# Performance work log

Measured on AMD Instinct MI355X. Metric: run time of the kernel, lower is better.

The kernel has to match this reference:

```python
import jax, jax.numpy as jnp
import numpy as np

B, S, D, H = 4, 2048, 1024, 16
HD = D // H  # head_dim = 64


def setup_inputs() -> dict:
    key = jax.random.key(0)
    k1, k2, k3 = jax.random.split(key, 3)
    x = jax.random.normal(k1, (B, S, D), dtype=jnp.float32)
    W_attn = jax.random.normal(k2, (D, 3 * D), dtype=jnp.float32) * (1.0 / np.sqrt(D))
    b_attn = jnp.zeros((3 * D,), dtype=jnp.float32)
    W_proj = jax.random.normal(k3, (D, D), dtype=jnp.float32) * (1.0 / np.sqrt(D))
    b_proj = jnp.zeros((D,), dtype=jnp.float32)
    return {"x": x, "W_attn": W_attn, "b_attn": b_attn, "W_proj": W_proj, "b_proj": b_proj}


def reference(x, W_attn, b_attn, W_proj, b_proj):
    bsz, seq_len, d = x.shape
    n_head = H
    head_dim = d // n_head
    qkv = x @ W_attn + b_attn                      # [B,S,3D]
    q, k, v = jnp.split(qkv, 3, axis=-1)           # each [B,S,D]
    # -> [B,H,S,hd]
    q = q.reshape(bsz, seq_len, n_head, head_dim).transpose(0, 2, 1, 3)
    k = k.reshape(bsz, seq_len, n_head, head_dim).transpose(0, 2, 1, 3)
    v = v.reshape(bsz, seq_len, n_head, head_dim).transpose(0, 2, 1, 3)
    scale = 1.0 / np.sqrt(head_dim).astype(np.float32)
    att = jnp.einsum("bhqd,bhkd->bhqk", q, k) * scale  # [B,H,S,S]
    causal = jnp.tril(jnp.ones((seq_len, seq_len), dtype=bool))
    att = jnp.where(causal[None, None], att, jnp.float32(-jnp.inf))
    att = jax.nn.softmax(att, axis=-1)
    y = jnp.einsum("bhqk,bhkd->bhqd", att, v)       # [B,H,S,hd]
    y = y.transpose(0, 2, 1, 3).reshape(bsz, seq_len, d)
    return y @ W_proj + b_proj
```

## Files before the change

kernel.cpp:

```cpp
#include <hip/hip_runtime.h>

typedef __attribute__((ext_vector_type(8))) short short8;
typedef __attribute__((ext_vector_type(8))) __bf16 bf16x8;
typedef __attribute__((ext_vector_type(2))) __bf16 bf16x2;
typedef __attribute__((ext_vector_type(4))) float f32x4;
typedef __attribute__((ext_vector_type(2))) unsigned int uint2v;

#define LOG2E 1.44269504088896340736f

__device__ __forceinline__ unsigned short f2b(float f) {
  unsigned u = __builtin_bit_cast(unsigned, f);
  u += 0x7fffu + ((u >> 16) & 1u);
  return (unsigned short)(u >> 16);
}
__device__ __forceinline__ float b2f(unsigned short s) {
  unsigned u = (unsigned)s << 16;
  return __builtin_bit_cast(float, u);
}
__device__ __forceinline__ bf16x8 asbf(short8 s) { return __builtin_bit_cast(bf16x8, s); }

__device__ __forceinline__ void gl_lds16(const void* g, void* l) {
  __builtin_amdgcn_global_load_lds(
      (const __attribute__((address_space(1))) void*)g,
      (__attribute__((address_space(3))) void*)l, 16, 0, 0);
}

__device__ __forceinline__ unsigned lds_a(const void* p) {
  return (unsigned)(size_t)(__attribute__((address_space(3))) const void*)p;
}

__device__ __forceinline__ unsigned pk_bf16(float a, float b) {
  bf16x2 v;
  v[0] = (__bf16)a;
  v[1] = (__bf16)b;
  return __builtin_bit_cast(unsigned, v);
}

template <int N>
__device__ __forceinline__ void wait_vm() {
  if constexpr (N == 7) asm volatile("s_waitcnt vmcnt(7)" ::: "memory");
  else if constexpr (N == 6) asm volatile("s_waitcnt vmcnt(6)" ::: "memory");
  else if constexpr (N == 5) asm volatile("s_waitcnt vmcnt(5)" ::: "memory");
  else asm volatile("s_waitcnt vmcnt(0)" ::: "memory");
}

__global__ void k_cvt_bf16(const float* __restrict__ x, unsigned short* __restrict__ o, int n) {
  int i = (blockIdx.x * 256 + threadIdx.x) * 4;
  if (i >= n) return;
  float4 v = *(const float4*)(x + i);
  ushort4 r;
  r.x = f2b(v.x); r.y = f2b(v.y); r.z = f2b(v.z); r.w = f2b(v.w);
  *(ushort4*)(o + i) = r;
}

__global__ void k_transpose_bf16(const float* __restrict__ W, unsigned short* __restrict__ Wt,
                                 int R, int C) {
  __shared__ float tile[64][65];
  const int tc = blockIdx.x, tr = blockIdx.y;
  const int r0 = tr * 64, c0 = tc * 64;
  for (int it = 0; it < 16; ++it) {
    int lin = it * 256 + threadIdx.x;
    int r = lin >> 6, c = lin & 63;
    tile[r][c] = W[(size_t)(r0 + r) * C + c0 + c];
  }
  __syncthreads();
  for (int it = 0; it < 16; ++it) {
    int lin = it * 256 + threadIdx.x;
    int orr = lin >> 6, oc = lin & 63;
    Wt[(size_t)(c0 + orr) * R + r0 + oc] = f2b(tile[oc][orr]);
  }
}

template <int BNW, bool OUT_BF16>
__global__ __launch_bounds__(512)
void k_gemm256(const unsigned short* __restrict__ A, const unsigned short* __restrict__ Bt,
               const float* __restrict__ bias, void* __restrict__ Cp,
               int M, int N, int K) {
  constexpr int BN = BNW * 4;
  constexpr int NR = BNW / 16;
  __shared__ unsigned short lds[2][(256 + BN) * 64];

  const int tid = threadIdx.x;
  const int wv = tid >> 6, lane = tid & 63;
  const int g = lane >> 4, l15 = lane & 15;
  const int wr = wv >> 2, wc = wv & 3;

  const int ntn = N / BN;
  const int nwg = gridDim.x;
  const int bid = blockIdx.x;
  const int cpx = nwg >> 3;
  const int swz = (bid & 7) * cpx + (bid >> 3);
  const int tm = swz / ntn, tn = swz % ntn;

  const unsigned short* Ab = A + (size_t)(tm * 256) * K;
  const unsigned short* Bb = Bt + (size_t)(tn * BN) * K;

  const int NT = K >> 6, NI = NT >> 1;

  auto As = [&](int buf) -> char* { return (char*)&lds[buf][0]; };
  auto Bs = [&](int buf) -> char* { return (char*)&lds[buf][256 * 64]; };

  auto stageB = [&](int buf, int t) {
#pragma unroll
    for (int it = 0; it < NR; ++it) {
      int cidx = it * 8 + wv;
      int row = cidx * 8 + (lane >> 3);
      int sc = (lane & 7) ^ (row & 7);
      gl_lds16(Bb + (size_t)row * K + t * 64 + sc * 8, Bs(buf) + cidx * 1024 + lane * 16);
    }
  };
  auto stageA = [&](int buf, int t, int q) {
    int row0 = (wv < 4) ? (q * 32 + wv * 8) : (128 + q * 32 + (wv - 4) * 8);
    int row = row0 + (lane >> 3);
    int sc = (lane & 7) ^ (row & 7);
    gl_lds16(Ab + (size_t)row * K + t * 64 + sc * 8, As(buf) + row0 * 128 + lane * 16);
  };

  auto rdA = [&](int buf, int q, int ms, int kh) -> short8 {
    int row = wr * 128 + q * 32 + ms * 16 + l15;
    int ch = (kh * 4 + g) ^ (row & 7);
    return *(const short8*)(As(buf) + row * 128 + ch * 16);
  };
  auto rdB = [&](int buf, int n, int kh) -> short8 {
    int row = wc * BNW + n * 16 + l15;
    int ch = (kh * 4 + g) ^ (row & 7);
    return *(const short8*)(Bs(buf) + row * 128 + ch * 16);
  };

  f32x4 acc[8][NR] = {};
  short8 bfr[NR][2];

  stageB(0, 0);
#pragma unroll
  for (int q = 0; q < 4; ++q) stageA(0, 0, q);
  stageB(1, 1);
#pragma unroll
  for (int q = 0; q < 3; ++q) stageA(1, 1, q);
  wait_vm<NR + 3>();
  __builtin_amdgcn_s_barrier();

  for (int i = 0; i < NI; ++i) {
    const int t0 = 2 * i;
#pragma unroll
    for (int half = 0; half < 2; ++half) {
#pragma unroll
      for (int q = 0; q < 4; ++q) {
        short8 afr[2][2];
#pragma unroll
        for (int ms = 0; ms < 2; ++ms)
#pragma unroll
          for (int kh = 0; kh < 2; ++kh) afr[ms][kh] = rdA(half, q, ms, kh);
        if (q == 0) {
#pragma unroll
          for (int n = 0; n < NR; ++n)
#pragma unroll
            for (int kh = 0; kh < 2; ++kh) bfr[n][kh] = rdB(half, n, kh);
        }
        if (half == 0) {
          if (q == 0) stageA(1, t0 + 1, 3);
          if (q == 1 && t0 + 2 < NT) { stageB(0, t0 + 2); stageA(0, t0 + 2, 0); }
          if (q == 2 && t0 + 2 < NT) stageA(0, t0 + 2, 1);
          if (q == 3 && t0 + 2 < NT) stageA(0, t0 + 2, 2);
        } else {
          if (q == 0 && t0 + 2 < NT) stageA(0, t0 + 2, 3);
          if (q == 1 && t0 + 3 < NT) stageB(1, t0 + 3);
          if (q == 2 && t0 + 3 < NT) stageA(1, t0 + 3, 0);
          if (q == 3 && t0 + 3 < NT) { stageA(1, t0 + 3, 1); stageA(1, t0 + 3, 2); }
        }
        __builtin_amdgcn_s_barrier();
        asm volatile("s_waitcnt lgkmcnt(0)" ::: "memory");
        __builtin_amdgcn_sched_barrier(0);
        __builtin_amdgcn_s_setprio(1);
#pragma unroll
        for (int n = 0; n < NR; ++n)
#pragma unroll
          for (int ms = 0; ms < 2; ++ms)
#pragma unroll
            for (int kh = 0; kh < 2; ++kh)
              acc[q * 2 + ms][n] = __builtin_amdgcn_mfma_f32_16x16x32_bf16(
                  asbf(afr[ms][kh]), asbf(bfr[n][kh]), acc[q * 2 + ms][n], 0, 0, 0);
        __builtin_amdgcn_s_setprio(0);
        if (q == 3) {
          const bool more = (half == 0) ? (t0 + 2 < NT) : (t0 + 3 < NT);
          if (more) wait_vm<NR + 3>();
          else      wait_vm<0>();
        }
        __builtin_amdgcn_s_barrier();
      }
    }
  }

  const int crow0 = tm * 256 + wr * 128 + g * 4;
  const int ccol0 = tn * BN + wc * BNW + l15;
#pragma unroll
  for (int n = 0; n < NR; ++n) {
    int col = ccol0 + n * 16;
    float bv = bias[col];
#pragma unroll
    for (int mq = 0; mq < 8; ++mq)
#pragma unroll
      for (int j = 0; j < 4; ++j) {
        int row = crow0 + mq * 16 + j;
        float v = acc[mq][n][j] + bv;
        if constexpr (OUT_BF16)
          ((unsigned short*)Cp)[(size_t)row * N + col] = f2b(v);
        else
          ((float*)Cp)[(size_t)row * N + col] = v;
      }
  }
}

__global__ __launch_bounds__(512)
void k_attn(const unsigned short* __restrict__ qkv, unsigned short* __restrict__ y) {
  constexpr int SEQ = 2048, TD = 3072, DM = 1024;
  __shared__ unsigned short Kl[2][4096];
  __shared__ unsigned short Vl[2][4096];
  __shared__ unsigned short Pl[8][2048];

  const int f = blockIdx.x;
  const int bh = (f & 7) * 8 + ((f >> 3) & 7);
  const int a = (f >> 6) & 7;
  const int qt = (f < 256) ? (7 - a) : (a - 4);
  const int b = bh >> 4, h = bh & 15;
  const int tid = threadIdx.x;
  const int lane = tid & 63, w = tid >> 6;
  const int g = lane >> 4, l15 = lane & 15;

  const size_t base = (size_t)b * SEQ * TD + h * 64;
  const unsigned short* Kg0 = qkv + base + 1024;
  const unsigned short* Vg0 = qkv + base + 2048;

  short8 onesb;
#pragma unroll
  for (int i = 0; i < 8; ++i) onesb[i] = (short)0x3F80;

  auto stage = [&](int buf, int c) {
    const unsigned short* Kg = Kg0 + (size_t)(c * 64) * TD;
    const unsigned short* Vg = Vg0 + (size_t)(c * 64) * TD;
    const int j = tid;
    int r = j >> 3, cc = j & 7;
    int cck = cc ^ (r & 7);
    gl_lds16(Kg + (size_t)r * TD + cck * 8, (char*)Kl[buf] + j * 16);
    int kv = ((j >> 1) & 3) | (((j >> 5) & 1) << 2) | (((j >> 3) & 3) << 3) |
             (((j >> 6) & 1) << 5);
    int d0 = ((j >> 7) << 4) | ((j & 1) << 3);
    gl_lds16(Vg + (size_t)kv * TD + d0, (char*)Vl[buf] + j * 16);
  };

  char* pw = (char*)Pl + w * 4096;

  const int q0 = qt * 256;
  const int qw = w * 32;

  short8 qf[2][2];
#pragma unroll
  for (int qg = 0; qg < 2; ++qg) {
    const unsigned short* qrow = qkv + base + (size_t)(q0 + qw + qg * 16 + l15) * TD;
#pragma unroll
    for (int kh = 0; kh < 2; ++kh) {
      short8 t = *(const short8*)(qrow + kh * 32 + g * 8);
#pragma unroll
      for (int i = 0; i < 8; ++i)
        t[i] = (short)f2b(b2f((unsigned short)t[i]) * (0.125f * LOG2E));
      qf[qg][kh] = t;
    }
  }

  f32x4 o[2][4] = {};
  f32x4 ol[2] = {};

  const int nch = 4 * (qt + 1);
  int cur = 0;
  stage(0, 0);
  for (int c = 0; c < nch; ++c) {
    if (c + 1 < nch) {
      stage(cur ^ 1, c + 1);
      asm volatile("s_waitcnt vmcnt(2)" ::: "memory");
    } else {
      asm volatile("s_waitcnt vmcnt(0)" ::: "memory");
    }
    __builtin_amdgcn_s_barrier();

    f32x4 sv[2][4];
    __builtin_amdgcn_s_setprio(1);
#pragma unroll
    for (int ff = 0; ff < 4; ++ff) {
      int kv = ff * 16 + l15;
      short8 kf0 = *(const short8*)((const char*)Kl[cur] + kv * 128 + ((g) ^ (kv & 7)) * 16);
      short8 kf1 = *(const short8*)((const char*)Kl[cur] + kv * 128 + ((4 + g) ^ (kv & 7)) * 16);
#pragma unroll
      for (int qg = 0; qg < 2; ++qg) {
        f32x4 s = {};
        s = __builtin_amdgcn_mfma_f32_16x16x32_bf16(asbf(kf0), asbf(qf[qg][0]), s, 0, 0, 0);
        s = __builtin_amdgcn_mfma_f32_16x16x32_bf16(asbf(kf1), asbf(qf[qg][1]), s, 0, 0, 0);
        sv[qg][ff] = s;
      }
    }
    __builtin_amdgcn_s_setprio(0);

    const int crel = c - 4 * qt;
    if (crel >= 0) {
#pragma unroll
      for (int qg = 0; qg < 2; ++qg)
#pragma unroll
        for (int ff = 0; ff < 4; ++ff)
#pragma unroll
          for (int r = 0; r < 4; ++r)
            if (crel * 64 + ff * 16 + g * 4 + r > qw + qg * 16 + l15)
              sv[qg][ff][r] = -128.f;
    }

#pragma unroll
    for (int qg = 0; qg < 2; ++qg)
#pragma unroll
      for (int ff = 0; ff < 4; ++ff) {
        float p0 = __builtin_amdgcn_exp2f(sv[qg][ff][0]);
        float p1 = __builtin_amdgcn_exp2f(sv[qg][ff][1]);
        float p2 = __builtin_amdgcn_exp2f(sv[qg][ff][2]);
        float p3 = __builtin_amdgcn_exp2f(sv[qg][ff][3]);
        unsigned w0 = pk_bf16(p0, p1);
        unsigned w1 = pk_bf16(p2, p3);
        unsigned long long pk = (unsigned long long)w0 | ((unsigned long long)w1 << 32);
        int off = qg * 2048 + ((l15 * 128 + ff * 32 + g * 8) ^ ((l15 & 7) << 4));
        *(unsigned long long*)(pw + off) = pk;
      }

    const unsigned vaddr = lds_a((const char*)Vl[cur] + g * 128 + l15 * 8);
#pragma unroll
    for (int kvh = 0; kvh < 2; ++kvh) {
      uint2v t0[4], t1[4];
#pragma unroll
      for (int n = 0; n < 4; ++n) {
        asm volatile("ds_read_b64_tr_b16 %0, %1 offset:%2"
                     : "=v"(t0[n]) : "v"(vaddr), "i"(n * 2048 + kvh * 1024));
        asm volatile("ds_read_b64_tr_b16 %0, %1 offset:%2"
                     : "=v"(t1[n]) : "v"(vaddr), "i"(n * 2048 + kvh * 1024 + 512));
      }
      asm volatile("s_waitcnt lgkmcnt(0)" ::: "memory");
      __builtin_amdgcn_sched_barrier(0);
      __builtin_amdgcn_s_setprio(1);
#pragma unroll
      for (int qg = 0; qg < 2; ++qg) {
        short8 pa = *(const short8*)(pw + qg * 2048 +
                                     ((l15 * 128 + kvh * 64 + g * 16) ^ ((l15 & 7) << 4)));
#pragma unroll
        for (int n = 0; n < 4; ++n) {
          union { uint2v u[2]; short8 s; } uu;
          uu.u[0] = t0[n]; uu.u[1] = t1[n];
          o[qg][n] = __builtin_amdgcn_mfma_f32_16x16x32_bf16(asbf(pa), asbf(uu.s),
                                                             o[qg][n], 0, 0, 0);
        }
        ol[qg] = __builtin_amdgcn_mfma_f32_16x16x32_bf16(asbf(pa), asbf(onesb),
                                                         ol[qg], 0, 0, 0);
      }
      __builtin_amdgcn_s_setprio(0);
    }

    __builtin_amdgcn_s_barrier();
    cur ^= 1;
  }

#pragma unroll
  for (int qg = 0; qg < 2; ++qg) {
    float lj[4];
#pragma unroll
    for (int j = 0; j < 4; ++j) lj[j] = 1.f / ol[qg][j];
#pragma unroll
    for (int n = 0; n < 4; ++n)
#pragma unroll
      for (int j = 0; j < 4; ++j) {
        int row = q0 + qw + qg * 16 + g * 4 + j;
        int col = h * 64 + n * 16 + l15;
        y[(size_t)(b * SEQ + row) * DM + col] = f2b(o[qg][n][j] * lj[j]);
      }
  }
}

extern "C" void kernel_launch(void* const* d_in, const int* in_sizes, int n_in,
                              void* d_out, int out_size, void* d_ws, size_t ws_size,
                              hipStream_t stream) {
  const float* x = (const float*)d_in[0];
  const float* W_attn = (const float*)d_in[1];
  const float* b_attn = (const float*)d_in[2];
  const float* W_proj = (const float*)d_in[3];
  const float* b_proj = (const float*)d_in[4];
  float* out = (float*)d_out;

  const int B = 4, S = 2048, D = 1024;
  const int M = B * S;
  const int TD = 3 * D;

  char* ws = (char*)d_ws;
  unsigned short* qkvb = (unsigned short*)ws;
  unsigned short* xb = (unsigned short*)(ws + (size_t)M * TD * 2);
  unsigned short* Wat = (unsigned short*)(ws + (size_t)M * TD * 2 + (size_t)M * D * 2);
  unsigned short* Wpt = Wat + (size_t)TD * D;

  k_cvt_bf16<<<(M * D) / 1024, 256, 0, stream>>>(x, xb, M * D);
  k_transpose_bf16<<<dim3(TD / 64, D / 64), 256, 0, stream>>>(W_attn, Wat, D, TD);
  k_transpose_bf16<<<dim3(D / 64, D / 64), 256, 0, stream>>>(W_proj, Wpt, D, D);

  k_gemm256<48, true><<<(M / 256) * (TD / 192), 512, 0, stream>>>(xb, Wat, b_attn, qkvb, M, TD, D);
  k_attn<<<512, 512, 0, stream>>>(qkvb, xb);
  k_gemm256<32, false><<<(M / 256) * (D / 128), 512, 0, stream>>>(xb, Wpt, b_proj, out, M, D, D);
}
```

Baseline: 162.5 us.

## Halve attention query tile to 128 rows with 256-thread blocks and 1024 blocks

The attention kernel now uses 4 waves per block, each block covering 128 query rows instead of 256, with twice as many blocks. Each thread issues two K/V LDS staging loads per chunk, the wait count moves to match, and the causal-tile scheduling is remapped so long and short tiles are interleaved across the grid. The aim is finer-grained work for better load balance across CUs and more resident blocks. The cost is that each K/V chunk is loaded from global memory once per block, so total K/V traffic roughly doubles.

```diff
diff --git a/kernel.cpp b/kernel.cpp
--- a/kernel.cpp
+++ b/kernel.cpp
@@ -41,6 +41,7 @@
   if constexpr (N == 7) asm volatile("s_waitcnt vmcnt(7)" ::: "memory");
   else if constexpr (N == 6) asm volatile("s_waitcnt vmcnt(6)" ::: "memory");
   else if constexpr (N == 5) asm volatile("s_waitcnt vmcnt(5)" ::: "memory");
+  else if constexpr (N == 4) asm volatile("s_waitcnt vmcnt(4)" ::: "memory");
   else asm volatile("s_waitcnt vmcnt(0)" ::: "memory");
 }
 
@@ -210,17 +211,17 @@
   }
 }
 
-__global__ __launch_bounds__(512)
+__global__ __launch_bounds__(256)
 void k_attn(const unsigned short* __restrict__ qkv, unsigned short* __restrict__ y) {
   constexpr int SEQ = 2048, TD = 3072, DM = 1024;
   __shared__ unsigned short Kl[2][4096];
   __shared__ unsigned short Vl[2][4096];
-  __shared__ unsigned short Pl[8][2048];
+  __shared__ unsigned short Pl[4][2048];
 
   const int f = blockIdx.x;
   const int bh = (f & 7) * 8 + ((f >> 3) & 7);
-  const int a = (f >> 6) & 7;
-  const int qt = (f < 256) ? (7 - a) : (a - 4);
+  const int s = (f >> 6) & 3, r4 = f >> 8;
+  const int qt = (r4 == 0) ? s : (r4 == 1) ? (15 - s) : (r4 == 2) ? (7 - s) : (8 + s);
   const int b = bh >> 4, h = bh & 15;
   const int tid = threadIdx.x;
   const int lane = tid & 63, w = tid >> 6;
@@ -237,19 +238,22 @@
   auto stage = [&](int buf, int c) {
     const unsigned short* Kg = Kg0 + (size_t)(c * 64) * TD;
     const unsigned short* Vg = Vg0 + (size_t)(c * 64) * TD;
-    const int j = tid;
-    int r = j >> 3, cc = j & 7;
-    int cck = cc ^ (r & 7);
-    gl_lds16(Kg + (size_t)r * TD + cck * 8, (char*)Kl[buf] + j * 16);
-    int kv = ((j >> 1) & 3) | (((j >> 5) & 1) << 2) | (((j >> 3) & 3) << 3) |
-             (((j >> 6) & 1) << 5);
-    int d0 = ((j >> 7) << 4) | ((j & 1) << 3);
-    gl_lds16(Vg + (size_t)kv * TD + d0, (char*)Vl[buf] + j * 16);
+#pragma unroll
+    for (int t = 0; t < 2; ++t) {
+      int j = t * 256 + tid;
+      int rr = j >> 3, cc = j & 7;
+      int cck = cc ^ (rr & 7);
+      gl_lds16(Kg + (size_t)rr * TD + cck * 8, (char*)Kl[buf] + j * 16);
+      int kv = ((j >> 1) & 3) | (((j >> 5) & 1) << 2) | (((j >> 3) & 3) << 3) |
+               (((j >> 6) & 1) << 5);
+      int d0 = ((j >> 7) << 4) | ((j & 1) << 3);
+      gl_lds16(Vg + (size_t)kv * TD + d0, (char*)Vl[buf] + j * 16);
+    }
   };
 
   char* pw = (char*)Pl + w * 4096;
 
-  const int q0 = qt * 256;
+  const int q0 = qt * 128;
   const int qw = w * 32;
 
   short8 qf[2][2];
@@ -269,13 +273,13 @@
   f32x4 o[2][4] = {};
   f32x4 ol[2] = {};
 
-  const int nch = 4 * (qt + 1);
+  const int nch = 2 * (qt + 1);
   int cur = 0;
   stage(0, 0);
   for (int c = 0; c < nch; ++c) {
     if (c + 1 < nch) {
       stage(cur ^ 1, c + 1);
-      asm volatile("s_waitcnt vmcnt(2)" ::: "memory");
+      asm volatile("s_waitcnt vmcnt(4)" ::: "memory");
     } else {
       asm volatile("s_waitcnt vmcnt(0)" ::: "memory");
     }
@@ -290,24 +294,24 @@
       short8 kf1 = *(const short8*)((const char*)Kl[cur] + kv * 128 + ((4 + g) ^ (kv & 7)) * 16);
 #pragma unroll
       for (int qg = 0; qg < 2; ++qg) {
-        f32x4 s = {};
-        s = __builtin_amdgcn_mfma_f32_16x16x32_bf16(asbf(kf0), asbf(qf[qg][0]), s, 0, 0, 0);
-        s = __builtin_amdgcn_mfma_f32_16x16x32_bf16(asbf(kf1), asbf(qf[qg][1]), s, 0, 0, 0);
-        sv[qg][ff] = s;
+        f32x4 sacc = {};
+        sacc = __builtin_amdgcn_mfma_f32_16x16x32_bf16(asbf(kf0), asbf(qf[qg][0]), sacc, 0, 0, 0);
+        sacc = __builtin_amdgcn_mfma_f32_16x16x32_bf16(asbf(kf1), asbf(qf[qg][1]), sacc, 0, 0, 0);
+        sv[qg][ff] = sacc;
       }
     }
     __builtin_amdgcn_s_setprio(0);
 
-    const int crel = c - 4 * qt;
+    const int crel = c - 2 * qt;
     if (crel >= 0) {
 #pragma unroll
       for (int qg = 0; qg < 2; ++qg)
 #pragma unroll
         for (int ff = 0; ff < 4; ++ff)
 #pragma unroll
-          for (int r = 0; r < 4; ++r)
-            if (crel * 64 + ff * 16 + g * 4 + r > qw + qg * 16 + l15)
-              sv[qg][ff][r] = -128.f;
+          for (int rr = 0; rr < 4; ++rr)
+            if (crel * 64 + ff * 16 + g * 4 + rr > qw + qg * 16 + l15)
+              sv[qg][ff][rr] = -128.f;
     }
 
 #pragma unroll
@@ -345,9 +349,9 @@
                                      ((l15 * 128 + kvh * 64 + g * 16) ^ ((l15 & 7) << 4)));
 #pragma unroll
         for (int n = 0; n < 4; ++n) {
-          union { uint2v u[2]; short8 s; } uu;
+          union { uint2v u[2]; short8 sv8; } uu;
           uu.u[0] = t0[n]; uu.u[1] = t1[n];
-          o[qg][n] = __builtin_amdgcn_mfma_f32_16x16x32_bf16(asbf(pa), asbf(uu.s),
+          o[qg][n] = __builtin_amdgcn_mfma_f32_16x16x32_bf16(asbf(pa), asbf(uu.sv8),
                                                              o[qg][n], 0, 0, 0);
         }
         ol[qg] = __builtin_amdgcn_mfma_f32_16x16x32_bf16(asbf(pa), asbf(onesb),
@@ -401,6 +405,6 @@
   k_transpose_bf16<<<dim3(D / 64, D / 64), 256, 0, stream>>>(W_proj, Wpt, D, D);
 
   k_gemm256<48, true><<<(M / 256) * (TD / 192), 512, 0, stream>>>(xb, Wat, b_attn, qkvb, M, TD, D);
-  k_attn<<<512, 512, 0, stream>>>(qkvb, xb);
+  k_attn<<<1024, 256, 0, stream>>>(qkvb, xb);
   k_gemm256<32, false><<<(M / 256) * (D / 128), 512, 0, stream>>>(xb, Wpt, b_proj, out, M, D, D);
 }
```

After: 173.2 us. +6.6%, slower.
